# Performance work log

Measured on AMD Instinct MI355X. Metric: run time of the kernel, lower is better.

The kernel has to match this reference:

```python
import jax, jax.numpy as jnp
import numpy as np

B, S, D, H = 16, 577, 1408, 16
HD = D // H  # 88


def setup_inputs() -> dict:
    key = jax.random.key(0)
    k1, k2, k3, k4, k5, k6 = jax.random.split(key, 6)
    hidden_states = jax.random.normal(k1, (B, S, D), dtype=jnp.float32)
    # realistic rotary table: cos/sin pairs stacked in last dim
    theta = jax.random.normal(k2, (S, HD // 2), dtype=jnp.float32)
    freqs_ci = jnp.stack([jnp.cos(theta), jnp.sin(theta)], axis=-1)  # (S, HD/2, 2)
    wqkv = jax.random.normal(k3, (3 * D, D), dtype=jnp.float32) * 0.02
    bqkv = jax.random.normal(k4, (3 * D,), dtype=jnp.float32) * 0.02
    wo = jax.random.normal(k5, (D, D), dtype=jnp.float32) * 0.02
    bo = jax.random.normal(k6, (D,), dtype=jnp.float32) * 0.02
    return {"hidden_states": hidden_states, "freqs_ci": freqs_ci,
            "wqkv": wqkv, "bqkv": bqkv, "wo": wo, "bo": bo}


def reference(hidden_states, freqs_ci, wqkv, bqkv, wo, bo):
    b, s, d = hidden_states.shape
    # fused QKV projection (torch Linear: x @ W.T + b)
    qkv = hidden_states @ wqkv.T + bqkv  # (B, S, 3D)
    q, k, v = jnp.split(qkv, 3, axis=-1)
    q = q.reshape(b, s, H, HD)
    k = k.reshape(b, s, H, HD)
    v = v.reshape(b, s, H, HD)

    cos = freqs_ci[..., 0][None, :, None, :]  # (1, S, 1, HD/2)
    sin = freqs_ci[..., 1][None, :, None, :]

    def rot(x):
        xr = x.reshape(b, s, H, HD // 2, 2)
        xe, xo = xr[..., 0], xr[..., 1]
        re = xe * cos - xo * sin
        ro = xe * sin + xo * cos
        return jnp.stack([re, ro], axis=-1).reshape(b, s, H, HD)

    q = rot(q)
    k = rot(k)

    scale = 1.0 / jnp.sqrt(jnp.float32(HD))  # SDPA default scaling
    scores = jnp.einsum('bqhd,bkhd->bhqk', q, k) * scale
    attn = jax.nn.softmax(scores, axis=-1)
    ctx = jnp.einsum('bhqk,bkhd->bqhd', attn, v).reshape(b, s, d)
    return ctx @ wo.T + bo
```

## Files before the change

### kernel.cpp

```cpp
#include <hip/hip_runtime.h>

typedef __attribute__((ext_vector_type(8))) __bf16 bf16x8;
typedef __attribute__((ext_vector_type(4))) float f32x4;
typedef __attribute__((ext_vector_type(4))) unsigned int uint4v;

#define B_ 16
#define S_ 577
#define D_ 1408
#define H_ 16
#define HD_ 88
#define MROWS (B_*S_)
#define N1 (3*D_)
#define K_ D_
#define KSTEPS 44
#define VT_LD 592
#define SCALE 0.10660035817780521f

static __device__ __forceinline__ void async16(void* lds, const void* g) {
  __builtin_amdgcn_global_load_lds((const __attribute__((address_space(1))) void*)g,
                                   (__attribute__((address_space(3))) void*)lds, 16, 0, 0);
}

static __device__ __forceinline__ int xcd_swizzle(int orig, int nwg) {
  int xcd = orig & 7, lid = orig >> 3;
  int q = nwg >> 3, r = nwg & 7;
  return (xcd < r ? xcd * (q + 1) : r * (q + 1) + (xcd - r) * q) + lid;
}

__global__ void cast_bf16_kernel(const float* __restrict__ src, __bf16* __restrict__ dst, int n4) {
  int i = blockIdx.x * blockDim.x + threadIdx.x;
  if (i >= n4) return;
  const float4 v = ((const float4*)src)[i];
  __bf16* d = dst + (size_t)i * 4;
  d[0] = (__bf16)v.x; d[1] = (__bf16)v.y; d[2] = (__bf16)v.z; d[3] = (__bf16)v.w;
}

__launch_bounds__(256, 2)
__global__ void gemm_qkv_rope(const __bf16* __restrict__ A, const __bf16* __restrict__ Bm,
                              const float* __restrict__ bias, const float* __restrict__ freqs,
                              __bf16* __restrict__ Qb, __bf16* __restrict__ Kb,
                              __bf16* __restrict__ Vb) {
  __shared__ __bf16 As[2][128 * 32];
  __shared__ __bf16 Bs[2][128 * 32];
  const int tid = threadIdx.x;
  const int w = tid >> 6, l = tid & 63;
  const int wgid = xcd_swizzle(blockIdx.x, 33 * 73);
  int mt, nt;
  if (wgid < 2376) { int bnd = wgid / 132, r = wgid % 132; nt = r >> 2; mt = bnd * 4 + (r & 3); }
  else             { nt = wgid - 2376; mt = 72; }
  const int m0 = mt * 128, n0 = nt * 128;
  const int wr = w & 1, wc = w >> 1;
  const int M = MROWS, K = K_;

  f32x4 acc[4][4];
#pragma unroll
  for (int m = 0; m < 4; ++m)
#pragma unroll
    for (int n = 0; n < 4; ++n) acc[m][n] = (f32x4){0.f, 0.f, 0.f, 0.f};

  int arow0 = m0 + w * 32 + (l >> 2);      if (arow0 >= M) arow0 = M - 1;
  int arow1 = m0 + w * 32 + 16 + (l >> 2); if (arow1 >= M) arow1 = M - 1;
  const __bf16* ag0 = A + (size_t)arow0 * K + (l & 3) * 8;
  const __bf16* ag1 = A + (size_t)arow1 * K + (l & 3) * 8;
  const __bf16* bg0 = Bm + (size_t)(n0 + w * 32 + (l >> 2)) * K + (l & 3) * 8;
  const __bf16* bg1 = Bm + (size_t)(n0 + w * 32 + 16 + (l >> 2)) * K + (l & 3) * 8;

  auto stage = [&](int buf, int k0) {
    async16(&As[buf][(w * 32) * 32],      ag0 + k0);
    async16(&As[buf][(w * 32 + 16) * 32], ag1 + k0);
    async16(&Bs[buf][(w * 32) * 32],      bg0 + k0);
    async16(&Bs[buf][(w * 32 + 16) * 32], bg1 + k0);
  };

  stage(0, 0);
  __syncthreads();
  for (int t = 0; t < KSTEPS; ++t) {
    const int cur = t & 1;
    if (t < KSTEPS - 1) stage(cur ^ 1, (t + 1) * 32);
    bf16x8 a[4], b[4];
#pragma unroll
    for (int m = 0; m < 4; ++m)
      a[m] = *(const bf16x8*)&As[cur][(wr * 64 + m * 16 + (l & 15)) * 32 + (l >> 4) * 8];
#pragma unroll
    for (int n = 0; n < 4; ++n)
      b[n] = *(const bf16x8*)&Bs[cur][(wc * 64 + n * 16 + (l & 15)) * 32 + (l >> 4) * 8];
#pragma unroll
    for (int m = 0; m < 4; ++m)
#pragma unroll
      for (int n = 0; n < 4; ++n)
        acc[m][n] = __builtin_amdgcn_mfma_f32_16x16x32_bf16(a[m], b[n], acc[m][n], 0, 0, 0);
    __syncthreads();
  }

  const int sect = n0 / 1408;
  __bf16* dst = (sect == 0) ? Qb : (sect == 1 ? Kb : Vb);
  int hN[4], dN[4], i2N[4];
  float bvN[4], sgnN[4];
#pragma unroll
  for (int n = 0; n < 4; ++n) {
    const int col = n0 + wc * 64 + n * 16 + (l & 15);
    const int cin = col - sect * 1408;
    hN[n] = cin / 88; dN[n] = cin - hN[n] * 88;
    bvN[n] = bias[col];
    i2N[n] = dN[n] & ~1;
    sgnN[n] = (dN[n] & 1) ? 1.f : -1.f;
  }
#pragma unroll
  for (int m = 0; m < 4; ++m) {
    const int rbase = m0 + wr * 64 + m * 16 + (l >> 4) * 4;
#pragma unroll
    for (int j = 0; j < 4; ++j) {
      const int r = rbase + j;
      const int s = r % 577;
      const int b = r / 577;
      const bool ok = r < MROWS;
      const float* frow = freqs + s * 88;
      __bf16* drow = dst + ((size_t)b * 16 * 577 + s) * 88;
#pragma unroll
      for (int n = 0; n < 4; ++n) {
        float val = acc[m][n][j] + bvN[n];
        float outv = val;
        if (sect < 2) {
          const float2 cs = *(const float2*)&frow[i2N[n]];
          const float p = __shfl_xor(val, 1);
          outv = val * cs.x + sgnN[n] * p * cs.y;
        }
        if (ok) drow[(size_t)hN[n] * 50776 + dN[n]] = (__bf16)outv;
      }
    }
  }
}

__launch_bounds__(256, 2)
__global__ void gemm_out_bias(const __bf16* __restrict__ A, const __bf16* __restrict__ Bm,
                              const float* __restrict__ bias, float* __restrict__ C) {
  __shared__ __bf16 As[2][128 * 32];
  __shared__ __bf16 Bs[2][128 * 32];
  const int tid = threadIdx.x;
  const int w = tid >> 6, l = tid & 63;
  const int wgid = xcd_swizzle(blockIdx.x, 11 * 73);
  int mt, nt;
  if (wgid < 792) { int bnd = wgid / 44, r = wgid % 44; nt = r >> 2; mt = bnd * 4 + (r & 3); }
  else            { nt = wgid - 792; mt = 72; }
  const int m0 = mt * 128, n0 = nt * 128;
  const int wr = w & 1, wc = w >> 1;
  const int M = MROWS, N = D_, K = K_;

  f32x4 acc[4][4];
#pragma unroll
  for (int m = 0; m < 4; ++m)
#pragma unroll
    for (int n = 0; n < 4; ++n) acc[m][n] = (f32x4){0.f, 0.f, 0.f, 0.f};

  int arow0 = m0 + w * 32 + (l >> 2);      if (arow0 >= M) arow0 = M - 1;
  int arow1 = m0 + w * 32 + 16 + (l >> 2); if (arow1 >= M) arow1 = M - 1;
  const __bf16* ag0 = A + (size_t)arow0 * K + (l & 3) * 8;
  const __bf16* ag1 = A + (size_t)arow1 * K + (l & 3) * 8;
  const __bf16* bg0 = Bm + (size_t)(n0 + w * 32 + (l >> 2)) * K + (l & 3) * 8;
  const __bf16* bg1 = Bm + (size_t)(n0 + w * 32 + 16 + (l >> 2)) * K + (l & 3) * 8;

  auto stage = [&](int buf, int k0) {
    async16(&As[buf][(w * 32) * 32],      ag0 + k0);
    async16(&As[buf][(w * 32 + 16) * 32], ag1 + k0);
    async16(&Bs[buf][(w * 32) * 32],      bg0 + k0);
    async16(&Bs[buf][(w * 32 + 16) * 32], bg1 + k0);
  };

  stage(0, 0);
  __syncthreads();
  for (int t = 0; t < KSTEPS; ++t) {
    const int cur = t & 1;
    if (t < KSTEPS - 1) stage(cur ^ 1, (t + 1) * 32);
    bf16x8 a[4], b[4];
#pragma unroll
    for (int m = 0; m < 4; ++m)
      a[m] = *(const bf16x8*)&As[cur][(wr * 64 + m * 16 + (l & 15)) * 32 + (l >> 4) * 8];
#pragma unroll
    for (int n = 0; n < 4; ++n)
      b[n] = *(const bf16x8*)&Bs[cur][(wc * 64 + n * 16 + (l & 15)) * 32 + (l >> 4) * 8];
#pragma unroll
    for (int m = 0; m < 4; ++m)
#pragma unroll
      for (int n = 0; n < 4; ++n)
        acc[m][n] = __builtin_amdgcn_mfma_f32_16x16x32_bf16(a[m], b[n], acc[m][n], 0, 0, 0);
    __syncthreads();
  }

#pragma unroll
  for (int n = 0; n < 4; ++n) {
    int col = n0 + wc * 64 + n * 16 + (l & 15);
    float bv = bias[col];
#pragma unroll
    for (int m = 0; m < 4; ++m) {
      int rbase = m0 + wr * 64 + m * 16 + (l >> 4) * 4;
#pragma unroll
      for (int j = 0; j < 4; ++j) {
        int r = rbase + j;
        if (r < MROWS) C[(size_t)r * N + col] = acc[m][n][j] + bv;
      }
    }
  }
}

__global__ void transpose_v(const __bf16* __restrict__ V, __bf16* __restrict__ Vt_g) {
  __shared__ __bf16 Ls[64 * 104];
  const int bh = blockIdx.x, t = blockIdx.y, s0 = t * 64;
  const int tid = threadIdx.x;
  const __bf16* vp = V + (size_t)bh * 577 * 88;
  for (int i = tid; i < 64 * 11; i += 256) {
    int r = i / 11, off = i % 11;
    int gs = s0 + r; if (gs > 576) gs = 576;
    *(uint4v*)&Ls[r * 104 + off * 8] = *(const uint4v*)(vp + (size_t)gs * 88 + off * 8);
  }
  __syncthreads();
  for (int i = tid; i < 88 * 8; i += 256) {
    int d = i / 8, so = (i % 8) * 8;
    int sc_ = s0 + so;
    if (sc_ < VT_LD) {
      __bf16 tmp[8];
#pragma unroll
      for (int j = 0; j < 8; ++j) tmp[j] = Ls[(so + j) * 104 + d];
      *(uint4v*)&Vt_g[((size_t)bh * 88 + d) * VT_LD + sc_] = *(uint4v*)tmp;
    }
  }
}

__launch_bounds__(256, 3)
__global__ void attn_kernel(const __bf16* __restrict__ Q, const __bf16* __restrict__ K,
                            const __bf16* __restrict__ Vt_gp, __bf16* __restrict__ ctx) {
  __shared__ __bf16 lds[26368];
  const int tid = threadIdx.x;
  const int w = tid >> 6, l = tid & 63;
  const int bh = blockIdx.x;
  const int q0 = blockIdx.y * 128;
  const __bf16* qp = Q + (size_t)bh * 577 * 88;
  const __bf16* kp = K + (size_t)bh * 577 * 88;
  const __bf16* vtp = Vt_gp + (size_t)bh * 88 * VT_LD;
  __bf16* Qs = lds;
  __bf16* Ks = lds + 12288;
  __bf16* Vt = lds + 17920;
  __bf16* Pw = lds + w * 2304;

  for (int i = tid; i < 128 * 11; i += 256) {
    int r = i / 11, off = i % 11;
    int gr = q0 + r; if (gr > 576) gr = 576;
    *(uint4v*)&Qs[r * 96 + off * 8] = *(const uint4v*)(qp + (size_t)gr * 88 + off * 8);
  }
  if (tid < 128) { uint4v z = 0; *(uint4v*)&Qs[tid * 96 + 88] = z; }
  __syncthreads();

  bf16x8 qf[2][3];
#pragma unroll
  for (int mg = 0; mg < 2; ++mg)
#pragma unroll
    for (int kk = 0; kk < 3; ++kk)
      qf[mg][kk] = *(const bf16x8*)&Qs[(w * 32 + mg * 16 + (l & 15)) * 96 + kk * 32 + (l >> 4) * 8];

  int preA[7], preB[7];
#pragma unroll
  for (int kch = 0; kch < 7; ++kch) {
    int c = w + 4 * kch;
    int a = 0, b2 = 0;
    if (c < 11) a = c * 512 + l * 8;
    else if (c < 27) { int e = (c - 11) * 512 + l * 8; a = (e / 88) * VT_LD; b2 = e % 88; }
    preA[kch] = a; preB[kch] = b2;
  }

  f32x4 oacc[2][6];
#pragma unroll
  for (int mg = 0; mg < 2; ++mg)
#pragma unroll
    for (int dn = 0; dn < 6; ++dn) oacc[mg][dn] = (f32x4){0.f, 0.f, 0.f, 0.f};
  f32x4 mrun[2], lrun[2];
  mrun[0] = -1e30f; mrun[1] = -1e30f;
  lrun[0] = 0.f; lrun[1] = 0.f;

  for (int t = 0; t < 10; ++t) {
    const int s0 = t * 64;
    if (t) __syncthreads();
#pragma unroll
    for (int kch = 0; kch < 7; ++kch) {
      int c = w + 4 * kch;
      if (c < 11) {
        async16(Ks + c * 512, kp + (size_t)s0 * 88 + preA[kch]);
      } else if (c < 27) {
        int g = s0 + preB[kch]; if (g > 584) g = 584;
        async16(Vt + (c - 11) * 512, vtp + preA[kch] + g);
      }
    }
    __syncthreads();

    f32x4 sc[2][4];
#pragma unroll
    for (int mg = 0; mg < 2; ++mg)
#pragma unroll
      for (int n = 0; n < 4; ++n) sc[mg][n] = (f32x4){0.f, 0.f, 0.f, 0.f};
#pragma unroll
    for (int n = 0; n < 4; ++n) {
#pragma unroll
      for (int kk = 0; kk < 3; ++kk) {
        bf16x8 kf = *(const bf16x8*)&Ks[(n * 16 + (l & 15)) * 88 + kk * 32 + (l >> 4) * 8];
        sc[0][n] = __builtin_amdgcn_mfma_f32_16x16x32_bf16(qf[0][kk], kf, sc[0][n], 0, 0, 0);
        sc[1][n] = __builtin_amdgcn_mfma_f32_16x16x32_bf16(qf[1][kk], kf, sc[1][n], 0, 0, 0);
      }
    }

    f32x4 tmax[2];
    tmax[0] = -1e30f; tmax[1] = -1e30f;
#pragma unroll
    for (int n = 0; n < 4; ++n) {
      const int kc = s0 + n * 16 + (l & 15);
      const bool valid = kc < 577;
#pragma unroll
      for (int mg = 0; mg < 2; ++mg)
#pragma unroll
        for (int j = 0; j < 4; ++j) {
          float v = valid ? sc[mg][n][j] * SCALE : -1e30f;
          sc[mg][n][j] = v;
          tmax[mg][j] = fmaxf(tmax[mg][j], v);
        }
    }
#pragma unroll
    for (int o = 1; o < 16; o <<= 1)
#pragma unroll
      for (int mg = 0; mg < 2; ++mg)
#pragma unroll
        for (int j = 0; j < 4; ++j)
          tmax[mg][j] = fmaxf(tmax[mg][j], __shfl_xor(tmax[mg][j], o));
#pragma unroll
    for (int mg = 0; mg < 2; ++mg)
#pragma unroll
      for (int j = 0; j < 4; ++j) {
        float mo = mrun[mg][j];
        float mn = fmaxf(mo, tmax[mg][j]);
        float sf = __expf(mo - mn);
        mrun[mg][j] = mn;
        lrun[mg][j] *= sf;
#pragma unroll
        for (int dn = 0; dn < 6; ++dn) oacc[mg][dn][j] *= sf;
      }
#pragma unroll
    for (int mg = 0; mg < 2; ++mg)
#pragma unroll
      for (int n = 0; n < 4; ++n)
#pragma unroll
        for (int j = 0; j < 4; ++j) {
          float p = __expf(sc[mg][n][j] - mrun[mg][j]);
          lrun[mg][j] += p;
          Pw[(mg * 16 + (l >> 4) * 4 + j) * 72 + n * 16 + (l & 15)] = (__bf16)p;
        }

#pragma unroll
    for (int ks = 0; ks < 2; ++ks) {
      bf16x8 pa0 = *(const bf16x8*)&Pw[((l & 15)) * 72 + ks * 32 + (l >> 4) * 8];
      bf16x8 pa1 = *(const bf16x8*)&Pw[(16 + (l & 15)) * 72 + ks * 32 + (l >> 4) * 8];
#pragma unroll
      for (int dn = 0; dn < 6; ++dn) {
        bf16x8 vb = *(const bf16x8*)&Vt[(dn * 16 + (l & 15)) * 88 + ks * 32 + (l >> 4) * 8];
        oacc[0][dn] = __builtin_amdgcn_mfma_f32_16x16x32_bf16(pa0, vb, oacc[0][dn], 0, 0, 0);
        oacc[1][dn] = __builtin_amdgcn_mfma_f32_16x16x32_bf16(pa1, vb, oacc[1][dn], 0, 0, 0);
      }
    }
  }

#pragma unroll
  for (int o = 1; o < 16; o <<= 1)
#pragma unroll
    for (int mg = 0; mg < 2; ++mg)
#pragma unroll
      for (int j = 0; j < 4; ++j)
        lrun[mg][j] += __shfl_xor(lrun[mg][j], o);

  const int b = bh >> 4, h = bh & 15;
#pragma unroll
  for (int mg = 0; mg < 2; ++mg) {
    float inv[4];
#pragma unroll
    for (int j = 0; j < 4; ++j) inv[j] = 1.f / lrun[mg][j];
    const int sqb = q0 + w * 32 + mg * 16 + (l >> 4) * 4;
#pragma unroll
    for (int dn = 0; dn < 6; ++dn) {
      const int d = dn * 16 + (l & 15);
      if (d >= 88) continue;
#pragma unroll
      for (int j = 0; j < 4; ++j) {
        const int sq = sqb + j;
        if (sq < 577)
          ctx[((size_t)(b * 577 + sq)) * 1408 + h * 88 + d] = (__bf16)(oacc[mg][dn][j] * inv[j]);
      }
    }
  }
}

extern "C" void kernel_launch(void* const* d_in, const int* in_sizes, int n_in,
                              void* d_out, int out_size, void* d_ws, size_t ws_size,
                              hipStream_t stream) {
  const float* hs    = (const float*)d_in[0];
  const float* freqs = (const float*)d_in[1];
  const float* wqkv  = (const float*)d_in[2];
  const float* bqkv  = (const float*)d_in[3];
  const float* wo    = (const float*)d_in[4];
  const float* bo    = (const float*)d_in[5];
  float* out = (float*)d_out;

  char* ws = (char*)d_ws;
  size_t off = 0;
  auto alloc = [&](size_t bytes) {
    void* p = ws + off;
    off += (bytes + 255) & ~(size_t)255;
    return p;
  };
  __bf16* x_bf    = (__bf16*)alloc((size_t)MROWS * K_ * 2);
  __bf16* ctx_bf  = x_bf;
  __bf16* wqkv_bf = (__bf16*)alloc((size_t)N1 * K_ * 2);
  __bf16* wo_bf   = (__bf16*)alloc((size_t)D_ * K_ * 2);
  __bf16* q_bf    = (__bf16*)alloc((size_t)MROWS * D_ * 2);
  __bf16* k_bf    = (__bf16*)alloc((size_t)MROWS * D_ * 2);
  __bf16* v_bf    = (__bf16*)alloc((size_t)MROWS * D_ * 2);
  __bf16* vt_g    = (__bf16*)d_out;

  cast_bf16_kernel<<<(MROWS * K_ / 4 + 255) / 256, 256, 0, stream>>>(hs, x_bf, MROWS * K_ / 4);
  cast_bf16_kernel<<<(N1 * K_ / 4 + 255) / 256, 256, 0, stream>>>(wqkv, wqkv_bf, N1 * K_ / 4);
  cast_bf16_kernel<<<(D_ * K_ / 4 + 255) / 256, 256, 0, stream>>>(wo, wo_bf, D_ * K_ / 4);

  gemm_qkv_rope<<<33 * 73, 256, 0, stream>>>(x_bf, wqkv_bf, bqkv, freqs, q_bf, k_bf, v_bf);

  transpose_v<<<dim3(256, 10), 256, 0, stream>>>(v_bf, vt_g);

  attn_kernel<<<dim3(256, 5), 256, 0, stream>>>(q_bf, k_bf, vt_g, ctx_bf);

  gemm_out_bias<<<11 * 73, 256, 0, stream>>>(ctx_bf, wo_bf, bo, out);
}
```

Measured before the change: 393.1 us.

## Fold softmax scale into Q, use exp2 with lazy rescaling, merge cast kernels

```diff
diff --git a/kernel.cpp b/kernel.cpp
--- a/kernel.cpp
+++ b/kernel.cpp
@@ -14,7 +14,7 @@
 #define K_ D_
 #define KSTEPS 44
 #define VT_LD 592
-#define SCALE 0.10660035817780521f
+#define QSCALE 0.15379180809f
 
 static __device__ __forceinline__ void async16(void* lds, const void* g) {
   __builtin_amdgcn_global_load_lds((const __attribute__((address_space(1))) void*)g,
@@ -27,12 +27,18 @@
   return (xcd < r ? xcd * (q + 1) : r * (q + 1) + (xcd - r) * q) + lid;
 }
 
-__global__ void cast_bf16_kernel(const float* __restrict__ src, __bf16* __restrict__ dst, int n4) {
+__global__ void cast3_bf16_kernel(const float* __restrict__ s0, __bf16* __restrict__ d0, int n0,
+                                  const float* __restrict__ s1, __bf16* __restrict__ d1, int n1,
+                                  const float* __restrict__ s2, __bf16* __restrict__ d2, int n2) {
   int i = blockIdx.x * blockDim.x + threadIdx.x;
-  if (i >= n4) return;
-  const float4 v = ((const float4*)src)[i];
-  __bf16* d = dst + (size_t)i * 4;
-  d[0] = (__bf16)v.x; d[1] = (__bf16)v.y; d[2] = (__bf16)v.z; d[3] = (__bf16)v.w;
+  const float* s; __bf16* d; int k;
+  if (i < n0) { s = s0; d = d0; k = i; }
+  else if (i < n0 + n1) { s = s1; d = d1; k = i - n0; }
+  else if (i < n0 + n1 + n2) { s = s2; d = d2; k = i - n0 - n1; }
+  else return;
+  const float4 v = ((const float4*)s)[k];
+  __bf16* p = d + (size_t)k * 4;
+  p[0] = (__bf16)v.x; p[1] = (__bf16)v.y; p[2] = (__bf16)v.z; p[3] = (__bf16)v.w;
 }
 
 __launch_bounds__(256, 2)
@@ -94,6 +100,7 @@
 
   const int sect = n0 / 1408;
   __bf16* dst = (sect == 0) ? Qb : (sect == 1 ? Kb : Vb);
+  const float qs = (sect == 0) ? QSCALE : 1.f;
   int hN[4], dN[4], i2N[4];
   float bvN[4], sgnN[4];
 #pragma unroll
@@ -123,7 +130,7 @@
         if (sect < 2) {
           const float2 cs = *(const float2*)&frow[i2N[n]];
           const float p = __shfl_xor(val, 1);
-          outv = val * cs.x + sgnN[n] * p * cs.y;
+          outv = (val * cs.x + sgnN[n] * p * cs.y) * qs;
         }
         if (ok) drow[(size_t)hN[n] * 50776 + dN[n]] = (__bf16)outv;
       }
@@ -315,7 +322,7 @@
       for (int mg = 0; mg < 2; ++mg)
 #pragma unroll
         for (int j = 0; j < 4; ++j) {
-          float v = valid ? sc[mg][n][j] * SCALE : -1e30f;
+          float v = valid ? sc[mg][n][j] : -1e30f;
           sc[mg][n][j] = v;
           tmax[mg][j] = fmaxf(tmax[mg][j], v);
         }
@@ -327,25 +334,34 @@
 #pragma unroll
         for (int j = 0; j < 4; ++j)
           tmax[mg][j] = fmaxf(tmax[mg][j], __shfl_xor(tmax[mg][j], o));
+
+    bool need = false;
 #pragma unroll
     for (int mg = 0; mg < 2; ++mg)
 #pragma unroll
-      for (int j = 0; j < 4; ++j) {
-        float mo = mrun[mg][j];
-        float mn = fmaxf(mo, tmax[mg][j]);
-        float sf = __expf(mo - mn);
-        mrun[mg][j] = mn;
-        lrun[mg][j] *= sf;
-#pragma unroll
-        for (int dn = 0; dn < 6; ++dn) oacc[mg][dn][j] *= sf;
-      }
+      for (int j = 0; j < 4; ++j)
+        need = need || (tmax[mg][j] > mrun[mg][j] + 8.f);
+    if (__any(need)) {
+#pragma unroll
+      for (int mg = 0; mg < 2; ++mg)
+#pragma unroll
+        for (int j = 0; j < 4; ++j) {
+          float mo = mrun[mg][j];
+          float mn = fmaxf(mo, tmax[mg][j]);
+          float sf = exp2f(mo - mn);
+          mrun[mg][j] = mn;
+          lrun[mg][j] *= sf;
+#pragma unroll
+          for (int dn = 0; dn < 6; ++dn) oacc[mg][dn][j] *= sf;
+        }
+    }
 #pragma unroll
     for (int mg = 0; mg < 2; ++mg)
 #pragma unroll
       for (int n = 0; n < 4; ++n)
 #pragma unroll
         for (int j = 0; j < 4; ++j) {
-          float p = __expf(sc[mg][n][j] - mrun[mg][j]);
+          float p = exp2f(sc[mg][n][j] - mrun[mg][j]);
           lrun[mg][j] += p;
           Pw[(mg * 16 + (l >> 4) * 4 + j) * 72 + n * 16 + (l & 15)] = (__bf16)p;
         }
@@ -419,9 +435,9 @@
   __bf16* v_bf    = (__bf16*)alloc((size_t)MROWS * D_ * 2);
   __bf16* vt_g    = (__bf16*)d_out;
 
-  cast_bf16_kernel<<<(MROWS * K_ / 4 + 255) / 256, 256, 0, stream>>>(hs, x_bf, MROWS * K_ / 4);
-  cast_bf16_kernel<<<(N1 * K_ / 4 + 255) / 256, 256, 0, stream>>>(wqkv, wqkv_bf, N1 * K_ / 4);
-  cast_bf16_kernel<<<(D_ * K_ / 4 + 255) / 256, 256, 0, stream>>>(wo, wo_bf, D_ * K_ / 4);
+  const int n0 = MROWS * K_ / 4, n1 = N1 * K_ / 4, n2 = D_ * K_ / 4;
+  cast3_bf16_kernel<<<(n0 + n1 + n2 + 255) / 256, 256, 0, stream>>>(
+      hs, x_bf, n0, wqkv, wqkv_bf, n1, wo, wo_bf, n2);
 
   gemm_qkv_rope<<<33 * 73, 256, 0, stream>>>(x_bf, wqkv_bf, bqkv, freqs, q_bf, k_bf, v_bf);
 
```

New measurement: 387.3 us (median of 3 runs). About the same (-1.5%).
